# Kernel tuning notes

Hardware: AMD Instinct MI355X
Metric: run time of the kernel (lower is better)

The kernel has to match this reference:

```python
import jax, jax.numpy as jnp
import numpy as np

IN_CHANNELS = 256
OUT_CHANNELS = 256
KERNEL_SIZE = 3
CHANNELS_PER_FILTER = 32
B, H, W = 4, 56, 56


def setup_inputs() -> dict:
    key = jax.random.key(0)
    k1, k2, k3 = jax.random.split(key, 3)
    x = jax.random.normal(k1, (B, IN_CHANNELS, H, W), dtype=jnp.float32)
    # kaiming-uniform-ish scale: bound = 1/sqrt(fan_in)
    fan_in = CHANNELS_PER_FILTER * KERNEL_SIZE ** 2
    bound = 1.0 / np.sqrt(fan_in)
    weight = jax.random.uniform(
        k2, (OUT_CHANNELS, CHANNELS_PER_FILTER, KERNEL_SIZE, KERNEL_SIZE),
        dtype=jnp.float32, minval=-bound, maxval=bound)
    connections = jax.random.randint(
        k3, (OUT_CHANNELS, CHANNELS_PER_FILTER), 0, IN_CHANNELS, dtype=jnp.int32)
    return {"x": x, "weight": weight, "connections": connections}


def reference(x, weight, connections):
    # x: (B, Cin, H, W); weight: (O, cpf, k, k); connections: (O, cpf) int32
    B_, O, cpf = x.shape[0], weight.shape[0], weight.shape[1]
    Hh, Ww = x.shape[2], x.shape[3]
    # Gather each filter's input-channel subset: (B, O, cpf, H, W)
    gathered = x[:, connections]
    # Grouped conv: each of the O groups convolves its cpf channels.
    gathered = gathered.reshape(B_, O * cpf, Hh, Ww)
    out = jax.lax.conv_general_dilated(
        gathered, weight,
        window_strides=(1, 1), padding="SAME",
        dimension_numbers=("NCHW", "OIHW", "NCHW"),
        feature_group_count=O)
    return out  # (B, O, H, W)
```

## Files before the change

### kernel.cpp

```cpp
#include <hip/hip_runtime.h>
#include <stdint.h>

#define NPIX 3136
#define OC 256
#define IC 256
#define CPF 32

__device__ __forceinline__ float dpp_shr1(float v) {
    return __int_as_float(__builtin_amdgcn_update_dpp(
        0, __float_as_int(v), 0x111, 0xF, 0xF, true));
}
__device__ __forceinline__ float dpp_shl1(float v) {
    return __int_as_float(__builtin_amdgcn_update_dpp(
        0, __float_as_int(v), 0x101, 0xF, 0xF, true));
}

__global__ __launch_bounds__(256, 4) void sparse_conv_kernel(
    const float* __restrict__ x, const float* __restrict__ weight,
    const int* __restrict__ connections, float* __restrict__ out)
{
    const int bid = blockIdx.x;
    const int b = bid & 3;
    const int o = bid >> 2;
    const int t = threadIdx.x;
    const int s = t & 15;
    const int g = t >> 4;
    const bool active = (g < 14);

    const float* xb   = x + (size_t)b * IC * NPIX;
    const int*   conn = connections + o * CPF;
    const float* wo   = weight + o * CPF * 9;

    int off[6]; bool mk[6];
#pragma unroll
    for (int k = 0; k < 6; ++k) {
        const int rr = 4 * g - 1 + k;
        const int rc = rr < 0 ? 0 : (rr > 55 ? 55 : rr);
        off[k] = rc * 56 + 4 * s;
        mk[k] = ((unsigned)rr < 56u) && active;
    }
    const bool redge = (s == 13);

    float4 acc[4];
#pragma unroll
    for (int r = 0; r < 4; ++r) acc[r] = make_float4(0.f, 0.f, 0.f, 0.f);

    auto loadrows = [&](int c, float4* m) {
        const float* plane = xb + (size_t)conn[c] * NPIX;
#pragma unroll
        for (int k = 0; k < 6; ++k)
            m[k] = *reinterpret_cast<const float4*>(plane + off[k]);
    };

    auto compute = [&](const float4* m, int c) {
        const float* wp = wo + c * 9;
        float wt[9];
#pragma unroll
        for (int i = 0; i < 9; ++i) wt[i] = wp[i];
#pragma unroll
        for (int k = 0; k < 6; ++k) {
            if (mk[k]) {
                const float4 mm = m[k];
                const float L = dpp_shr1(mm.w);
                float       R = dpp_shl1(mm.x);
                R = redge ? 0.f : R;
#pragma unroll
                for (int r = 0; r < 4; ++r) {
                    const int kh = k - r;
                    if (kh >= 0 && kh < 3) {
                        const float w0 = wt[kh * 3 + 0];
                        const float w1 = wt[kh * 3 + 1];
                        const float w2 = wt[kh * 3 + 2];
                        acc[r].x += w0 * L    + w1 * mm.x + w2 * mm.y;
                        acc[r].y += w0 * mm.x + w1 * mm.y + w2 * mm.z;
                        acc[r].z += w0 * mm.y + w1 * mm.z + w2 * mm.w;
                        acc[r].w += w0 * mm.z + w1 * mm.w + w2 * R;
                    }
                }
            }
        }
    };

    float4 mA[6], mB[6];
    loadrows(0, mA);
#pragma unroll 1
    for (int it = 0; it < 16; ++it) {
        const int c = 2 * it;
        loadrows(c + 1, mB);
        compute(mA, c);
        if (it < 15) loadrows(c + 2, mA);
        compute(mB, c + 1);
    }

    if (active && s < 14) {
        float* ob = out + ((size_t)b * OC + o) * NPIX + (4 * g) * 56 + 4 * s;
#pragma unroll
        for (int r = 0; r < 4; ++r)
            *reinterpret_cast<float4*>(ob + r * 56) = acc[r];
    }
}

extern "C" void kernel_launch(void* const* d_in, const int* in_sizes, int n_in,
                              void* d_out, int out_size, void* d_ws, size_t ws_size,
                              hipStream_t stream) {
    const float* x    = (const float*)d_in[0];
    const float* wgt  = (const float*)d_in[1];
    const int*   conn = (const int*)d_in[2];
    float* out = (float*)d_out;

    dim3 grid(4 * OC);
    dim3 block(256);
    hipLaunchKernelGGL(sparse_conv_kernel, grid, block, 0, stream, x, wgt, conn, out);
}
```

Baseline: 114.8 us.

## Convert inputs to fp16 and use packed fdot2 for channel-pair accumulation

Adds pre-pass kernels that convert x to fp16 and pack weights into channel-pair half2 words. The main kernel loads two gathered channels at once as half data, interleaves them with perm, and accumulates with v_dot2 fp16 instructions into fp32, halving gather bandwidth and FMA count. It adds two extra launches and a full read/write pass over x, and reduces input precision to fp16, which may affect accuracy tolerance.

```diff
diff --git a/kernel.cpp b/kernel.cpp
--- a/kernel.cpp
+++ b/kernel.cpp
@@ -5,18 +5,49 @@
 #define OC 256
 #define IC 256
 #define CPF 32
+#define XH_BYTES 6422528
 
-__device__ __forceinline__ float dpp_shr1(float v) {
-    return __int_as_float(__builtin_amdgcn_update_dpp(
-        0, __float_as_int(v), 0x111, 0xF, 0xF, true));
+typedef _Float16 h2_t __attribute__((ext_vector_type(2)));
+
+__device__ __forceinline__ uint32_t pk16(float lo, float hi) {
+    uint16_t l = __builtin_bit_cast(uint16_t, (_Float16)lo);
+    uint16_t h = __builtin_bit_cast(uint16_t, (_Float16)hi);
+    return (uint32_t)l | ((uint32_t)h << 16);
 }
-__device__ __forceinline__ float dpp_shl1(float v) {
-    return __int_as_float(__builtin_amdgcn_update_dpp(
-        0, __float_as_int(v), 0x101, 0xF, 0xF, true));
+__device__ __forceinline__ float fdot2(uint32_t w, uint32_t xp, float acc) {
+    return __builtin_amdgcn_fdot2(__builtin_bit_cast(h2_t, w),
+                                  __builtin_bit_cast(h2_t, xp), acc, false);
+}
+__device__ __forceinline__ uint32_t dpp_shr1(uint32_t v) {
+    return (uint32_t)__builtin_amdgcn_update_dpp(0, (int)v, 0x111, 0xF, 0xF, true);
+}
+__device__ __forceinline__ uint32_t dpp_shl1(uint32_t v) {
+    return (uint32_t)__builtin_amdgcn_update_dpp(0, (int)v, 0x101, 0xF, 0xF, true);
+}
+
+__global__ __launch_bounds__(256) void cvt_x(const float* __restrict__ x,
+                                             uint32_t* __restrict__ xh) {
+    const int i = blockIdx.x * 256 + threadIdx.x;
+    const float4 a = ((const float4*)x)[2 * i];
+    const float4 b = ((const float4*)x)[2 * i + 1];
+    uint4 o;
+    o.x = pk16(a.x, a.y); o.y = pk16(a.z, a.w);
+    o.z = pk16(b.x, b.y); o.w = pk16(b.z, b.w);
+    ((uint4*)xh)[i] = o;
+}
+
+__global__ __launch_bounds__(256) void cvt_w(const float* __restrict__ w,
+                                             uint32_t* __restrict__ wp) {
+    const int i = blockIdx.x * 256 + threadIdx.x;
+    const int o = i / 144, rem = i - o * 144;
+    const int cc = rem / 9, kd = rem - cc * 9;
+    const float w0 = w[(o * CPF + 2 * cc) * 9 + kd];
+    const float w1 = w[(o * CPF + 2 * cc + 1) * 9 + kd];
+    wp[i] = pk16(w0, w1);
 }
 
 __global__ __launch_bounds__(256, 4) void sparse_conv_kernel(
-    const float* __restrict__ x, const float* __restrict__ weight,
+    const uint16_t* __restrict__ xh, const uint32_t* __restrict__ wp,
     const int* __restrict__ connections, float* __restrict__ out)
 {
     const int bid = blockIdx.x;
@@ -26,70 +57,76 @@
     const int s = t & 15;
     const int g = t >> 4;
     const bool active = (g < 14);
+    const bool redge = (s == 13);
 
-    const float* xb   = x + (size_t)b * IC * NPIX;
-    const int*   conn = connections + o * CPF;
-    const float* wo   = weight + o * CPF * 9;
+    const int* conn = connections + o * CPF;
+    const uint32_t* wo = wp + o * 144;
 
     int off[6]; bool mk[6];
+    const int col = (4 * s > 52) ? 52 : 4 * s;
 #pragma unroll
     for (int k = 0; k < 6; ++k) {
         const int rr = 4 * g - 1 + k;
         const int rc = rr < 0 ? 0 : (rr > 55 ? 55 : rr);
-        off[k] = rc * 56 + 4 * s;
+        off[k] = rc * 56 + col;
         mk[k] = ((unsigned)rr < 56u) && active;
     }
-    const bool redge = (s == 13);
 
     float4 acc[4];
 #pragma unroll
     for (int r = 0; r < 4; ++r) acc[r] = make_float4(0.f, 0.f, 0.f, 0.f);
 
-    auto loadrows = [&](int c, float4* m) {
-        const float* plane = xb + (size_t)conn[c] * NPIX;
+    auto loadpair = [&](int cc, uint2* A, uint2* B) {
+        const uint16_t* p0 = xh + ((size_t)b * IC + conn[2 * cc]) * NPIX;
+        const uint16_t* p1 = xh + ((size_t)b * IC + conn[2 * cc + 1]) * NPIX;
 #pragma unroll
-        for (int k = 0; k < 6; ++k)
-            m[k] = *reinterpret_cast<const float4*>(plane + off[k]);
+        for (int k = 0; k < 6; ++k) {
+            A[k] = *reinterpret_cast<const uint2*>(p0 + off[k]);
+            B[k] = *reinterpret_cast<const uint2*>(p1 + off[k]);
+        }
     };
 
-    auto compute = [&](const float4* m, int c) {
-        const float* wp = wo + c * 9;
-        float wt[9];
+    auto compute = [&](const uint2* A, const uint2* B, int cc) {
+        uint32_t wt[9];
+        const uint32_t* w9 = wo + cc * 9;
 #pragma unroll
-        for (int i = 0; i < 9; ++i) wt[i] = wp[i];
+        for (int i = 0; i < 9; ++i) wt[i] = w9[i];
 #pragma unroll
         for (int k = 0; k < 6; ++k) {
             if (mk[k]) {
-                const float4 mm = m[k];
-                const float L = dpp_shr1(mm.w);
-                float       R = dpp_shl1(mm.x);
-                R = redge ? 0.f : R;
+                const uint32_t I0 = __builtin_amdgcn_perm(A[k].x, B[k].x, 0x01000504u);
+                const uint32_t I1 = __builtin_amdgcn_perm(A[k].x, B[k].x, 0x03020706u);
+                const uint32_t I2 = __builtin_amdgcn_perm(A[k].y, B[k].y, 0x01000504u);
+                const uint32_t I3 = __builtin_amdgcn_perm(A[k].y, B[k].y, 0x03020706u);
+                const uint32_t Lp = dpp_shr1(I3);
+                uint32_t       Rp = dpp_shl1(I0);
+                Rp = redge ? 0u : Rp;
 #pragma unroll
                 for (int r = 0; r < 4; ++r) {
                     const int kh = k - r;
                     if (kh >= 0 && kh < 3) {
-                        const float w0 = wt[kh * 3 + 0];
-                        const float w1 = wt[kh * 3 + 1];
-                        const float w2 = wt[kh * 3 + 2];
-                        acc[r].x += w0 * L    + w1 * mm.x + w2 * mm.y;
-                        acc[r].y += w0 * mm.x + w1 * mm.y + w2 * mm.z;
-                        acc[r].z += w0 * mm.y + w1 * mm.z + w2 * mm.w;
-                        acc[r].w += w0 * mm.z + w1 * mm.w + w2 * R;
+                        const uint32_t w0 = wt[kh * 3 + 0];
+                        const uint32_t w1 = wt[kh * 3 + 1];
+                        const uint32_t w2 = wt[kh * 3 + 2];
+                        acc[r].x = fdot2(w2, I1, fdot2(w1, I0, fdot2(w0, Lp, acc[r].x)));
+                        acc[r].y = fdot2(w2, I2, fdot2(w1, I1, fdot2(w0, I0, acc[r].y)));
+                        acc[r].z = fdot2(w2, I3, fdot2(w1, I2, fdot2(w0, I1, acc[r].z)));
+                        acc[r].w = fdot2(w2, Rp, fdot2(w1, I3, fdot2(w0, I2, acc[r].w)));
                     }
                 }
             }
         }
     };
 
-    float4 mA[6], mB[6];
-    loadrows(0, mA);
+    uint2 A0[6], B0[6], A1[6], B1[6];
+    loadpair(0, A0, B0);
 #pragma unroll 1
-    for (int it = 0; it < 16; ++it) {
-        const int c = 2 * it;
-        loadrows(c + 1, mB);
-        compute(mA, c);
-        if (it < 15) loadrows(c + 2, mA);
-        compute(mB, c + 1);
+    for (int it = 0; it < 8; ++it) {
+        const int cc = 2 * it;
+        loadpair(cc + 1, A1, B1);
+        compute(A0, B0, cc);
+        if (it < 7) loadpair(cc + 2, A0, B0);
+        compute(A1, B1, cc + 1);
     }
 
     if (active && s < 14) {
@@ -108,7 +145,11 @@
     const int*   conn = (const int*)d_in[2];
     float* out = (float*)d_out;
 
-    dim3 grid(4 * OC);
-    dim3 block(256);
-    hipLaunchKernelGGL(sparse_conv_kernel, grid, block, 0, stream, x, wgt, conn, out);
+    uint32_t* xh = (uint32_t*)d_ws;
+    uint32_t* wp = (uint32_t*)((char*)d_ws + XH_BYTES);
+
+    hipLaunchKernelGGL(cvt_x, dim3(1568), dim3(256), 0, stream, x, xh);
+    hipLaunchKernelGGL(cvt_w, dim3(144),  dim3(256), 0, stream, wgt, wp);
+    hipLaunchKernelGGL(sparse_conv_kernel, dim3(4 * OC), dim3(256), 0, stream,
+                       (const uint16_t*)xh, wp, conn, out);
 }
```

Result: faster. 101.1 us (-12.0%).
